# Kernel tuning notes

Hardware: AMD Instinct MI355X
Metric: run time of the kernel (lower is better)

Reference implementation:

```python
import jax, jax.numpy as jnp
import numpy as np
import math

R, C, B, E = 64, 256, 1, 768
H, DK, F = 8, 96, 3072
EPS = 1e-5


def _ln(x, w, b):
    m = jnp.mean(x, axis=-1, keepdims=True)
    v = jnp.var(x, axis=-1, keepdims=True)
    return (x - m) / jnp.sqrt(v + EPS) * w + b


def _lin(x, w, b):
    # torch Linear: y = x @ W^T + b, W: [out, in]
    return jnp.einsum('...i,oi->...o', x, w) + b


def setup_inputs() -> dict:
    key = jax.random.key(0)
    ks = jax.random.split(key, 16)
    w = lambda k, s: jax.random.normal(k, s, dtype=jnp.float32) * 0.02
    z = lambda s: jnp.zeros(s, dtype=jnp.float32)
    o = lambda s: jnp.ones(s, dtype=jnp.float32)
    return {
        'x': jax.random.normal(ks[0], (R, C, B, E), dtype=jnp.float32),
        'ln_row_w': o((E,)), 'ln_row_b': z((E,)),
        'row_q_w': w(ks[1], (E, E)), 'row_q_b': z((E,)),
        'row_k_w': w(ks[2], (E, E)), 'row_k_b': z((E,)),
        'row_v_w': w(ks[3], (E, E)), 'row_v_b': z((E,)),
        'row_o_w': w(ks[4], (E, E)), 'row_o_b': z((E,)),
        'ln_col_w': o((E,)), 'ln_col_b': z((E,)),
        'col_q_w': w(ks[5], (E, E)), 'col_q_b': z((E,)),
        'col_k_w': w(ks[6], (E, E)), 'col_k_b': z((E,)),
        'col_v_w': w(ks[7], (E, E)), 'col_v_b': z((E,)),
        'col_o_w': w(ks[8], (E, E)), 'col_o_b': z((E,)),
        'ln_ffn_w': o((E,)), 'ln_ffn_b': z((E,)),
        'fc1_w': w(ks[9], (F, E)), 'fc1_b': z((F,)),
        'fc2_w': w(ks[10], (E, F)), 'fc2_b': z((E,)),
    }


def reference(x, ln_row_w, ln_row_b, row_q_w, row_q_b, row_k_w, row_k_b,
              row_v_w, row_v_b, row_o_w, row_o_b,
              ln_col_w, ln_col_b, col_q_w, col_q_b, col_k_w, col_k_b,
              col_v_w, col_v_b, col_o_w, col_o_b,
              ln_ffn_w, ln_ffn_b, fc1_w, fc1_b, fc2_w, fc2_b):
    r, c, n, e = x.shape  # n_rows, n_cols, batch, embed

    # ---- Row self-attention (pre-LN residual block) ----
    xn = _ln(x, ln_row_w, ln_row_b)
    scaling = (DK ** -0.5) / math.sqrt(r)  # align_scaling: extra 1/sqrt(n_rows)
    q = _lin(xn, row_q_w, row_q_b).reshape(r, c, n, H, DK) * scaling
    k = _lin(xn, row_k_w, row_k_b).reshape(r, c, n, H, DK)
    v = _lin(xn, row_v_w, row_v_b).reshape(r, c, n, H, DK)
    row_logits = jnp.einsum('rinhd,rjnhd->hnij', q, k)  # sums over rows
    row_probs = jax.nn.softmax(row_logits, axis=-1)     # [H, B, C, C]
    rc = jnp.einsum('hnij,rjnhd->rinhd', row_probs, v).reshape(r, c, n, e)
    x = x + _lin(rc, row_o_w, row_o_b)

    # ---- Column self-attention (pre-LN residual block) ----
    xn = _ln(x, ln_col_w, ln_col_b)
    q = _lin(xn, col_q_w, col_q_b).reshape(r, c, n, H, DK) * (DK ** -0.5)
    k = _lin(xn, col_k_w, col_k_b).reshape(r, c, n, H, DK)
    v = _lin(xn, col_v_w, col_v_b).reshape(r, c, n, H, DK)
    col_logits = jnp.einsum('icnhd,jcnhd->hcnij', q, k)
    col_probs = jax.nn.softmax(col_logits, axis=-1)     # [H, C, B, R, R]
    cc = jnp.einsum('hcnij,jcnhd->icnhd', col_probs, v).reshape(r, c, n, e)
    x = x + _lin(cc, col_o_w, col_o_b)

    # ---- Feed-forward (pre-LN residual block) ----
    xn = _ln(x, ln_ffn_w, ln_ffn_b)
    h = jax.nn.gelu(_lin(xn, fc1_w, fc1_b), approximate=False)
    x = x + _lin(h, fc2_w, fc2_b)

    return x, row_probs, col_probs
```

## Files before the change

kernel.cpp:

```cpp
#include <hip/hip_runtime.h>
#include <cstdint>

typedef unsigned short u16;
typedef __attribute__((ext_vector_type(8))) short short8;
typedef __attribute__((ext_vector_type(4))) short short4v;
typedef __attribute__((ext_vector_type(4))) float floatx4;

#define DEV __device__ __forceinline__

DEV float bf2f(u16 u) { union { uint32_t i; float f; } w; w.i = ((uint32_t)u) << 16; return w.f; }
DEV u16 f2bf(float f) {
  union { float f; uint32_t i; } w; w.f = f;
  uint32_t x = w.i;
  return (u16)((x + 0x7fffu + ((x >> 16) & 1u)) >> 16);
}

DEV void async_copy16(const u16* g, u16* l) {
  __builtin_amdgcn_global_load_lds(
      (const __attribute__((address_space(1))) void*)(uintptr_t)g,
      (__attribute__((address_space(3))) void*)(uint32_t)(uintptr_t)l,
      16, 0, 0);
}

__global__ __launch_bounds__(256) void cvt(const float* __restrict__ s,
                                           u16* __restrict__ d, int n) {
  const int i = (blockIdx.x * 256 + threadIdx.x) * 4;
  if (i >= n) return;
  floatx4 f = *(const floatx4*)(s + i);
  short4v o;
#pragma unroll
  for (int j = 0; j < 4; ++j) o[j] = (short)f2bf(f[j]);
  *(short4v*)(d + i) = o;
}

template<bool INF32>
__global__ __launch_bounds__(256) void ln_kernel(const void* __restrict__ in,
                                                 const float* __restrict__ w,
                                                 const float* __restrict__ b,
                                                 u16* __restrict__ out) {
  const int wid = threadIdx.x >> 6, lane = threadIdx.x & 63;
  const int row = blockIdx.x * 4 + wid;
  const size_t base = (size_t)row * 768;
  float v[12];
#pragma unroll
  for (int p = 0; p < 3; ++p) {
    const int e = p * 256 + lane * 4;
    if constexpr (INF32) {
      floatx4 f = *(const floatx4*)((const float*)in + base + e);
#pragma unroll
      for (int j = 0; j < 4; ++j) v[p * 4 + j] = f[j];
    } else {
      short4v u = *(const short4v*)((const u16*)in + base + e);
#pragma unroll
      for (int j = 0; j < 4; ++j) v[p * 4 + j] = bf2f((u16)u[j]);
    }
  }
  float s = 0.f, sq = 0.f;
#pragma unroll
  for (int i = 0; i < 12; ++i) { s += v[i]; sq += v[i] * v[i]; }
#pragma unroll
  for (int m = 1; m < 64; m <<= 1) { s += __shfl_xor(s, m); sq += __shfl_xor(sq, m); }
  const float mean = s * (1.f / 768.f);
  const float var = sq * (1.f / 768.f) - mean * mean;
  const float rstd = rsqrtf(var + 1e-5f);
#pragma unroll
  for (int p = 0; p < 3; ++p) {
    const int e = p * 256 + lane * 4;
    floatx4 wv = *(const floatx4*)(w + e);
    floatx4 bv = *(const floatx4*)(b + e);
    short4v o;
#pragma unroll
    for (int j = 0; j < 4; ++j) {
      float y = (v[p * 4 + j] - mean) * rstd * wv[j] + bv[j];
      o[j] = (short)f2bf(y);
    }
    *(short4v*)(out + base + e) = o;
  }
}

template<int AMODE, int EPI>
__global__ __launch_bounds__(256) void gemm_bt(
    const u16* __restrict__ A, const u16* __restrict__ B,
    const float* __restrict__ bias, const void* __restrict__ res,
    void* __restrict__ out, int K, int lda, int ldb,
    long long aBatch, long long bBatch, long long outBatch, int ldc, float scale) {
  __shared__ u16 lA[128 * 32];
  __shared__ u16 lB[128 * 32];
  const int t = threadIdx.x;
  const int z = blockIdx.z;
  const int m0 = blockIdx.x * 128, n0 = blockIdx.y * 128;
  const u16* Ab;
  const u16* Bb;
  int koff = 0;
  if constexpr (AMODE == 0) { Ab = A + (size_t)z * aBatch; Bb = B + (size_t)z * bBatch; }
  else if constexpr (AMODE == 1) { Ab = A + z * 96; Bb = B + z * 96; }
  else { const int h = z >> 4; Ab = A + h * 96; Bb = B + h * 96; koff = (z & 15) * 384; }

  const int krow = t >> 2;
  const int kcol = (t & 3) << 3;
  const int wid = t >> 6, lane = t & 63;
  const int wr = wid >> 1, wc = wid & 1;
  const int lrow = lane & 15, lhi = lane >> 4;

  floatx4 acc[4][4];
#pragma unroll
  for (int i = 0; i < 4; ++i)
#pragma unroll
    for (int j = 0; j < 4; ++j) acc[i][j] = (floatx4){0.f, 0.f, 0.f, 0.f};

  for (int k0 = 0; k0 < K; k0 += 32) {
#pragma unroll
    for (int i = 0; i < 2; ++i) {
      const int row = i * 64 + krow;
      const int kk = koff + k0 + kcol;
      const u16 *ga, *gb;
      if constexpr (AMODE == 0) {
        ga = Ab + (size_t)(m0 + row) * lda + kk;
        gb = Bb + (size_t)(n0 + row) * ldb + kk;
      } else {
        const int r = kk / 96, d = kk - r * 96;
        ga = Ab + (size_t)r * 196608 + (size_t)(m0 + row) * 768 + d;
        gb = Bb + (size_t)r * 196608 + (size_t)(n0 + row) * 768 + d;
      }
      async_copy16(ga, lA + i * 2048 + wid * 512);
      async_copy16(gb, lB + i * 2048 + wid * 512);
    }
    asm volatile("s_waitcnt vmcnt(0)" ::: "memory");
    __syncthreads();

    short8 af[4], bfr[4];
#pragma unroll
    for (int mi = 0; mi < 4; ++mi)
      af[mi] = *(const short8*)&lA[(wr * 64 + mi * 16 + lrow) * 32 + lhi * 8];
#pragma unroll
    for (int ni = 0; ni < 4; ++ni)
      bfr[ni] = *(const short8*)&lB[(wc * 64 + ni * 16 + lrow) * 32 + lhi * 8];
#pragma unroll
    for (int mi = 0; mi < 4; ++mi)
#pragma unroll
      for (int ni = 0; ni < 4; ++ni)
        acc[mi][ni] = __builtin_amdgcn_mfma_f32_16x16x32_bf16(af[mi], bfr[ni], acc[mi][ni], 0, 0, 0);
    __syncthreads();
  }

  const int mbase = m0 + wr * 64;
  const int nbase = n0 + wc * 64;
#pragma unroll
  for (int mi = 0; mi < 4; ++mi) {
#pragma unroll
    for (int ni = 0; ni < 4; ++ni) {
      const int n = nbase + ni * 16 + lrow;
      float bz = 0.f;
      if constexpr (EPI != 1 && EPI != 7) { if (bias) bz = bias[n]; }
#pragma unroll
      for (int r4 = 0; r4 < 4; ++r4) {
        const int m = mbase + mi * 16 + lhi * 4 + r4;
        const float val = acc[mi][ni][r4];
        if constexpr (EPI == 0) {
          ((u16*)out)[(size_t)z * outBatch + (size_t)m * ldc + n] = f2bf((val + bz) * scale);
        } else if constexpr (EPI == 1) {
          ((float*)out)[(size_t)z * outBatch + (size_t)m * ldc + n] = val;
        } else if constexpr (EPI == 2) {
          const float x = val + bz;
          ((u16*)out)[(size_t)m * ldc + n] = f2bf(0.5f * x * (1.f + erff(x * 0.70710678118f)));
        } else if constexpr (EPI == 3) {
          const float r = ((const float*)res)[(size_t)m * ldc + n];
          ((float*)out)[(size_t)m * ldc + n] = r + val + bz;
        } else if constexpr (EPI == 4) {
          const float r = ((const float*)res)[(size_t)m * ldc + n];
          ((u16*)out)[(size_t)m * ldc + n] = f2bf(r + val + bz);
        } else if constexpr (EPI == 5) {
          const float r = bf2f(((const u16*)res)[(size_t)m * ldc + n]);
          ((float*)out)[(size_t)m * ldc + n] = r + val + bz;
        } else if constexpr (EPI == 6) {
          const float r = bf2f(((const u16*)res)[(size_t)m * ldc + n]);
          ((u16*)out)[(size_t)m * ldc + n] = f2bf(r + val + bz);
        } else if constexpr (EPI == 7) {
          const int rr = n / 96, d = n - rr * 96;
          ((u16*)out)[((size_t)(rr * 256 + m)) * 768 + (size_t)z * 96 + d] = f2bf(val);
        }
      }
    }
  }
}

__global__ __launch_bounds__(256) void softmax_row(const float* __restrict__ part,
                                                   float* __restrict__ probs_f,
                                                   u16* __restrict__ probs_b) {
  const int wid = threadIdx.x >> 6, lane = threadIdx.x & 63;
  const int row = blockIdx.x * 4 + wid;
  const int h = row >> 8, i = row & 255;
  const size_t base = (size_t)h * 16 * 65536 + (size_t)i * 256 + lane * 4;
  floatx4 v = (floatx4){0.f, 0.f, 0.f, 0.f};
#pragma unroll
  for (int s16 = 0; s16 < 16; ++s16) {
    floatx4 p = *(const floatx4*)(part + base + (size_t)s16 * 65536);
#pragma unroll
    for (int j = 0; j < 4; ++j) v[j] += p[j];
  }
  float mx = fmaxf(fmaxf(v[0], v[1]), fmaxf(v[2], v[3]));
#pragma unroll
  for (int m = 1; m < 64; m <<= 1) mx = fmaxf(mx, __shfl_xor(mx, m));
  float e[4], s = 0.f;
#pragma unroll
  for (int j = 0; j < 4; ++j) { e[j] = __expf(v[j] - mx); s += e[j]; }
#pragma unroll
  for (int m = 1; m < 64; m <<= 1) s += __shfl_xor(s, m);
  const float inv = 1.f / s;
  floatx4 of;
  short4v ob;
#pragma unroll
  for (int j = 0; j < 4; ++j) {
    const float p = e[j] * inv;
    of[j] = p;
    ob[j] = (short)f2bf(p);
  }
  *(floatx4*)(probs_f + (size_t)row * 256 + lane * 4) = of;
  *(short4v*)(probs_b + (size_t)row * 256 + lane * 4) = ob;
}

__global__ __launch_bounds__(256) void pack_vt(const u16* __restrict__ v, u16* __restrict__ vt) {
  __shared__ u16 S[64][104];
  const int jb = blockIdx.x, r = blockIdx.y, h = blockIdx.z;
  const int t = threadIdx.x;
#pragma unroll
  for (int p = 0; p < 3; ++p) {
    const int cid = t + p * 256;
    const int j = cid / 12, ch = cid - j * 12;
    short8 x = *(const short8*)&v[((size_t)(r * 256 + jb * 64 + j)) * 768 + h * 96 + ch * 8];
    *(short8*)&S[j][ch * 8] = x;
  }
  __syncthreads();
#pragma unroll
  for (int p = 0; p < 3; ++p) {
    const int cid = t + p * 256;
    const int d = cid / 8, cj = cid - d * 8;
    u16 tmp[8];
#pragma unroll
    for (int m = 0; m < 8; ++m) tmp[m] = S[cj * 8 + m][d];
    *(short8*)&vt[((size_t)(h * 6144 + r * 96 + d)) * 256 + jb * 64 + cj * 8] = *(short8*)tmp;
  }
}

__global__ __launch_bounds__(256) void col_attn(const u16* __restrict__ q,
                                                const u16* __restrict__ k,
                                                const u16* __restrict__ v,
                                                float* __restrict__ probs,
                                                u16* __restrict__ ctx) {
  __shared__ u16 qs[64][104];
  __shared__ u16 ks[64][104];
  __shared__ u16 vt[96][72];
  __shared__ u16 ps[64][72];
  const int c = blockIdx.x, h = blockIdx.y;
  const int t = threadIdx.x;
#pragma unroll
  for (int p = 0; p < 3; ++p) {
    const int cid = t + p * 256;
    const int i = cid / 12, ch = cid - i * 12;
    const size_t g = ((size_t)(i * 256 + c)) * 768 + h * 96 + ch * 8;
    short8 qv = *(const short8*)(q + g);
    short8 kv = *(const short8*)(k + g);
    short8 vv = *(const short8*)(v + g);
    *(short8*)&qs[i][ch * 8] = qv;
    *(short8*)&ks[i][ch * 8] = kv;
#pragma unroll
    for (int m = 0; m < 8; ++m) vt[ch * 8 + m][i] = (u16)vv[m];
  }
  __syncthreads();
  const int lane = t & 63, wid = t >> 6;
  const int lrow = lane & 15, lhi = lane >> 4;

  floatx4 s[4];
#pragma unroll
  for (int nj = 0; nj < 4; ++nj) s[nj] = (floatx4){0.f, 0.f, 0.f, 0.f};
#pragma unroll
  for (int kk = 0; kk < 3; ++kk) {
    short8 a = *(const short8*)&qs[wid * 16 + lrow][kk * 32 + lhi * 8];
#pragma unroll
    for (int nj = 0; nj < 4; ++nj) {
      short8 bb = *(const short8*)&ks[nj * 16 + lrow][kk * 32 + lhi * 8];
      s[nj] = __builtin_amdgcn_mfma_f32_16x16x32_bf16(a, bb, s[nj], 0, 0, 0);
    }
  }
  const size_t pb = ((size_t)(h * 256 + c)) * 4096;
#pragma unroll
  for (int r4 = 0; r4 < 4; ++r4) {
    float mx = fmaxf(fmaxf(s[0][r4], s[1][r4]), fmaxf(s[2][r4], s[3][r4]));
    mx = fmaxf(mx, __shfl_xor(mx, 1));
    mx = fmaxf(mx, __shfl_xor(mx, 2));
    mx = fmaxf(mx, __shfl_xor(mx, 4));
    mx = fmaxf(mx, __shfl_xor(mx, 8));
    float e[4], sum = 0.f;
#pragma unroll
    for (int nj = 0; nj < 4; ++nj) { e[nj] = __expf(s[nj][r4] - mx); sum += e[nj]; }
    sum += __shfl_xor(sum, 1);
    sum += __shfl_xor(sum, 2);
    sum += __shfl_xor(sum, 4);
    sum += __shfl_xor(sum, 8);
    const float inv = 1.f / sum;
    const int i = wid * 16 + lhi * 4 + r4;
#pragma unroll
    for (int nj = 0; nj < 4; ++nj) {
      const float pv = e[nj] * inv;
      const int j = nj * 16 + lrow;
      probs[pb + (size_t)i * 64 + j] = pv;
      ps[i][j] = f2bf(pv);
    }
  }
  __syncthreads();
  floatx4 o[6];
#pragma unroll
  for (int df = 0; df < 6; ++df) o[df] = (floatx4){0.f, 0.f, 0.f, 0.f};
#pragma unroll
  for (int k2 = 0; k2 < 2; ++k2) {
    short8 a = *(const short8*)&ps[wid * 16 + lrow][k2 * 32 + lhi * 8];
#pragma unroll
    for (int df = 0; df < 6; ++df) {
      short8 bb = *(const short8*)&vt[df * 16 + lrow][k2 * 32 + lhi * 8];
      o[df] = __builtin_amdgcn_mfma_f32_16x16x32_bf16(a, bb, o[df], 0, 0, 0);
    }
  }
#pragma unroll
  for (int df = 0; df < 6; ++df)
#pragma unroll
    for (int r4 = 0; r4 < 4; ++r4) {
      const int i = wid * 16 + lhi * 4 + r4;
      const int d = df * 16 + lrow;
      ctx[((size_t)(i * 256 + c)) * 768 + h * 96 + d] = f2bf(o[df][r4]);
    }
}

extern "C" void kernel_launch(void* const* d_in, const int* in_sizes, int n_in,
                              void* d_out, int out_size, void* d_ws, size_t ws_size,
                              hipStream_t stream) {
  const float* x_in  = (const float*)d_in[0];
  const float* lnr_w = (const float*)d_in[1];
  const float* lnr_b = (const float*)d_in[2];
  const float* rq_w  = (const float*)d_in[3];
  const float* rq_b  = (const float*)d_in[4];
  const float* rk_w  = (const float*)d_in[5];
  const float* rk_b  = (const float*)d_in[6];
  const float* rv_w  = (const float*)d_in[7];
  const float* rv_b  = (const float*)d_in[8];
  const float* ro_w  = (const float*)d_in[9];
  const float* ro_b  = (const float*)d_in[10];
  const float* lnc_w = (const float*)d_in[11];
  const float* lnc_b = (const float*)d_in[12];
  const float* cq_w  = (const float*)d_in[13];
  const float* cq_b  = (const float*)d_in[14];
  const float* ck_w  = (const float*)d_in[15];
  const float* ck_b  = (const float*)d_in[16];
  const float* cv_w  = (const float*)d_in[17];
  const float* cv_b  = (const float*)d_in[18];
  const float* co_w  = (const float*)d_in[19];
  const float* co_b  = (const float*)d_in[20];
  const float* lnf_w = (const float*)d_in[21];
  const float* lnf_b = (const float*)d_in[22];
  const float* f1_w  = (const float*)d_in[23];
  const float* f1_b  = (const float*)d_in[24];
  const float* f2_w  = (const float*)d_in[25];
  const float* f2_b  = (const float*)d_in[26];

  char* ws = (char*)d_ws;
  const size_t WSZ_E = 589824 * 2;
  u16* w_rq = (u16*)ws;
  u16* w_rk = (u16*)(ws + WSZ_E);
  u16* w_rv = (u16*)(ws + 2 * WSZ_E);
  u16* w_ro = (u16*)(ws + 3 * WSZ_E);
  u16* w_cq = (u16*)(ws + 4 * WSZ_E);
  u16* w_ck = (u16*)(ws + 5 * WSZ_E);
  u16* w_cv = (u16*)(ws + 6 * WSZ_E);
  u16* w_co = (u16*)(ws + 7 * WSZ_E);
  u16* w_f1 = (u16*)(ws + 8 * WSZ_E);
  u16* w_f2 = (u16*)(ws + 8 * WSZ_E + 4718592);
  size_t off = 8 * WSZ_E + 2 * 4718592;

  const bool xf32 = ws_size >= 147849216ULL;
  char* x_cur = ws + off;
  off += xf32 ? 50331648 : 25165824;
  u16* qb = (u16*)(ws + off); off += 25165824;
  u16* kb = (u16*)(ws + off); off += 25165824;
  u16* vb = (u16*)(ws + off); off += 25165824;
  u16* probsb = (u16*)(ws + off);

  u16* vt     = qb;
  u16* ctx1   = kb;
  u16* hidden = qb;
  u16* xn3    = vb;

  float* out_x  = (float*)d_out;
  float* out_rp = out_x + 12582912;
  float* out_cp = out_x + 13107200;
  u16* xn   = (u16*)out_x;
  u16* ctx2 = (u16*)((char*)out_x + 25165824);
  float* part = out_x;

  const dim3 blk(256);
  const float s_row = 0.0127577591f;
  const float s_col = 0.1020620726f;

  cvt<<<576, blk, 0, stream>>>(rq_w, w_rq, 589824);
  cvt<<<576, blk, 0, stream>>>(rk_w, w_rk, 589824);
  cvt<<<576, blk, 0, stream>>>(rv_w, w_rv, 589824);
  cvt<<<576, blk, 0, stream>>>(ro_w, w_ro, 589824);
  cvt<<<576, blk, 0, stream>>>(cq_w, w_cq, 589824);
  cvt<<<576, blk, 0, stream>>>(ck_w, w_ck, 589824);
  cvt<<<576, blk, 0, stream>>>(cv_w, w_cv, 589824);
  cvt<<<576, blk, 0, stream>>>(co_w, w_co, 589824);
  cvt<<<2304, blk, 0, stream>>>(f1_w, w_f1, 2359296);
  cvt<<<2304, blk, 0, stream>>>(f2_w, w_f2, 2359296);

  ln_kernel<true><<<4096, blk, 0, stream>>>(x_in, lnr_w, lnr_b, xn);
  gemm_bt<0, 0><<<dim3(128, 6, 1), blk, 0, stream>>>(xn, w_rq, rq_b, nullptr, qb, 768, 768, 768, 0, 0, 0, 768, s_row);
  gemm_bt<0, 0><<<dim3(128, 6, 1), blk, 0, stream>>>(xn, w_rk, rk_b, nullptr, kb, 768, 768, 768, 0, 0, 0, 768, 1.f);
  gemm_bt<0, 0><<<dim3(128, 6, 1), blk, 0, stream>>>(xn, w_rv, rv_b, nullptr, vb, 768, 768, 768, 0, 0, 0, 768, 1.f);
  gemm_bt<2, 1><<<dim3(2, 2, 128), blk, 0, stream>>>(qb, kb, nullptr, nullptr, part, 384, 0, 0, 0, 0, 65536LL, 256, 1.f);
  softmax_row<<<512, blk, 0, stream>>>(part, out_rp, probsb);
  pack_vt<<<dim3(4, 64, 8), blk, 0, stream>>>(vb, vt);
  gemm_bt<0, 7><<<dim3(2, 48, 8), blk, 0, stream>>>(probsb, vt, nullptr, nullptr, ctx1, 256, 256, 256, 65536LL, 1572864LL, 0, 0, 1.f);
  if (xf32)
    gemm_bt<0, 3><<<dim3(128, 6, 1), blk, 0, stream>>>(ctx1, w_ro, ro_b, x_in, x_cur, 768, 768, 768, 0, 0, 0, 768, 1.f);
  else
    gemm_bt<0, 4><<<dim3(128, 6, 1), blk, 0, stream>>>(ctx1, w_ro, ro_b, x_in, x_cur, 768, 768, 768, 0, 0, 0, 768, 1.f);

  if (xf32) ln_kernel<true><<<4096, blk, 0, stream>>>(x_cur, lnc_w, lnc_b, xn);
  else      ln_kernel<false><<<4096, blk, 0, stream>>>(x_cur, lnc_w, lnc_b, xn);
  gemm_bt<0, 0><<<dim3(128, 6, 1), blk, 0, stream>>>(xn, w_cq, cq_b, nullptr, qb, 768, 768, 768, 0, 0, 0, 768, s_col);
  gemm_bt<0, 0><<<dim3(128, 6, 1), blk, 0, stream>>>(xn, w_ck, ck_b, nullptr, kb, 768, 768, 768, 0, 0, 0, 768, 1.f);
  gemm_bt<0, 0><<<dim3(128, 6, 1), blk, 0, stream>>>(xn, w_cv, cv_b, nullptr, vb, 768, 768, 768, 0, 0, 0, 768, 1.f);
  col_attn<<<dim3(256, 8), blk, 0, stream>>>(qb, kb, vb, out_cp, ctx2);
  if (xf32)
    gemm_bt<0, 3><<<dim3(128, 6, 1), blk, 0, stream>>>(ctx2, w_co, co_b, x_cur, x_cur, 768, 768, 768, 0, 0, 0, 768, 1.f);
  else
    gemm_bt<0, 6><<<dim3(128, 6, 1), blk, 0, stream>>>(ctx2, w_co, co_b, x_cur, x_cur, 768, 768, 768, 0, 0, 0, 768, 1.f);

  if (xf32) ln_kernel<true><<<4096, blk, 0, stream>>>(x_cur, lnf_w, lnf_b, xn3);
  else      ln_kernel<false><<<4096, blk, 0, stream>>>(x_cur, lnf_w, lnf_b, xn3);
  gemm_bt<0, 2><<<dim3(128, 12, 1), blk, 0, stream>>>(xn3, w_f1, f1_b, nullptr, hidden, 768, 768, 768, 0, 0, 0, 1536, 1.f);
  if (xf32)
    gemm_bt<0, 3><<<dim3(128, 6, 1), blk, 0, stream>>>(hidden, w_f2, f2_b, x_cur, out_x, 1536, 1536, 3072, 0, 0, 0, 768, 1.f);
  else
    gemm_bt<0, 5><<<dim3(128, 6, 1), blk, 0, stream>>>(hidden, w_f2, f2_b, x_cur, out_x, 1536, 1536, 3072, 0, 0, 0, 768, 1.f);
  gemm_bt<0, 2><<<dim3(128, 12, 1), blk, 0, stream>>>(xn3, w_f1 + 1536 * 768, f1_b + 1536, nullptr, hidden, 768, 768, 768, 0, 0, 0, 1536, 1.f);
  gemm_bt<0, 3><<<dim3(128, 6, 1), blk, 0, stream>>>(hidden, w_f2 + 1536, nullptr, out_x, out_x, 1536, 1536, 3072, 0, 0, 0, 768, 1.f);
}
```

Before: 703.6 us.

## Fuse QKV GEMMs, merge weight conversions, widen GEMM K-tile, use fast GELU

Merges the ten weight-conversion launches into one kernel and folds the query scaling into the converted Q weights and packed biases. Replaces the three separate Q/K/V projection GEMMs with one wide GEMM (N=2304) whose epilogue scatters results into the q/k/v buffers. Doubles the GEMM K-tile from 32 to 64, halving the barriers per K step at the cost of twice the LDS. Swaps erff in the GELU epilogue for a polynomial approximation with fast exp, which slightly changes numerics.

Result: slower. 828.6 us (+17.8%).

```diff
diff --git a/kernel.cpp b/kernel.cpp
--- a/kernel.cpp
+++ b/kernel.cpp
@@ -15,6 +15,17 @@
   return (u16)((x + 0x7fffu + ((x >> 16) & 1u)) >> 16);
 }
 
+DEV float fast_gelu(float x) {
+  const float y = x * 0.70710678118f;
+  const float ay = fabsf(y);
+  const float t = 1.f / (1.f + 0.3275911f * ay);
+  const float poly = t * (0.254829592f + t * (-0.284496736f +
+                     t * (1.421413741f + t * (-1.453152027f + t * 1.061405429f))));
+  const float er = 1.f - poly * __expf(-y * y);
+  const float erf_y = __builtin_copysignf(er, y);
+  return 0.5f * x * (1.f + erf_y);
+}
+
 DEV void async_copy16(const u16* g, u16* l) {
   __builtin_amdgcn_global_load_lds(
       (const __attribute__((address_space(1))) void*)(uintptr_t)g,
@@ -22,15 +33,34 @@
       16, 0, 0);
 }
 
-__global__ __launch_bounds__(256) void cvt(const float* __restrict__ s,
-                                           u16* __restrict__ d, int n) {
-  const int i = (blockIdx.x * 256 + threadIdx.x) * 4;
-  if (i >= n) return;
-  floatx4 f = *(const floatx4*)(s + i);
+struct CvtArgs {
+  const float* src[10];
+  float scale[10];
+};
+__global__ __launch_bounds__(256) void cvt_all(CvtArgs a, u16* __restrict__ dst) {
+  const size_t e = ((size_t)blockIdx.x * 256 + threadIdx.x) * 4;
+  if (e >= 9437184) return;
+  int reg;
+  size_t base;
+  if (e < 4718592) { reg = (int)(e / 589824); base = (size_t)reg * 589824; }
+  else if (e < 7077888) { reg = 8; base = 4718592; }
+  else { reg = 9; base = 7077888; }
+  const float sc = a.scale[reg];
+  floatx4 f = *(const floatx4*)(a.src[reg] + (e - base));
   short4v o;
 #pragma unroll
-  for (int j = 0; j < 4; ++j) o[j] = (short)f2bf(f[j]);
-  *(short4v*)(d + i) = o;
+  for (int j = 0; j < 4; ++j) o[j] = (short)f2bf(f[j] * sc);
+  *(short4v*)(dst + e) = o;
+}
+
+__global__ __launch_bounds__(256) void bias_pack(const float* __restrict__ qb,
+                                                 const float* __restrict__ kb,
+                                                 const float* __restrict__ vb,
+                                                 float sq, float* __restrict__ out) {
+  const int i = blockIdx.x * 256 + threadIdx.x;
+  if (i >= 2304) return;
+  const int buf = i / 768, c = i - buf * 768;
+  out[i] = buf == 0 ? qb[c] * sq : (buf == 1 ? kb[c] : vb[c]);
 }
 
 template<bool INF32>
@@ -84,8 +114,8 @@
     const float* __restrict__ bias, const void* __restrict__ res,
     void* __restrict__ out, int K, int lda, int ldb,
     long long aBatch, long long bBatch, long long outBatch, int ldc, float scale) {
-  __shared__ u16 lA[128 * 32];
-  __shared__ u16 lB[128 * 32];
+  __shared__ u16 lA[128 * 64];
+  __shared__ u16 lB[128 * 64];
   const int t = threadIdx.x;
   const int z = blockIdx.z;
   const int m0 = blockIdx.x * 128, n0 = blockIdx.y * 128;
@@ -96,8 +126,8 @@
   else if constexpr (AMODE == 1) { Ab = A + z * 96; Bb = B + z * 96; }
   else { const int h = z >> 4; Ab = A + h * 96; Bb = B + h * 96; koff = (z & 15) * 384; }
 
-  const int krow = t >> 2;
-  const int kcol = (t & 3) << 3;
+  const int srow = t >> 3;
+  const int scol = (t & 7) << 3;
   const int wid = t >> 6, lane = t & 63;
   const int wr = wid >> 1, wc = wid & 1;
   const int lrow = lane & 15, lhi = lane >> 4;
@@ -108,11 +138,11 @@
 #pragma unroll
     for (int j = 0; j < 4; ++j) acc[i][j] = (floatx4){0.f, 0.f, 0.f, 0.f};
 
-  for (int k0 = 0; k0 < K; k0 += 32) {
-#pragma unroll
-    for (int i = 0; i < 2; ++i) {
-      const int row = i * 64 + krow;
-      const int kk = koff + k0 + kcol;
+  for (int k0 = 0; k0 < K; k0 += 64) {
+#pragma unroll
+    for (int p = 0; p < 4; ++p) {
+      const int row = p * 32 + srow;
+      const int kk = koff + k0 + scol;
       const u16 *ga, *gb;
       if constexpr (AMODE == 0) {
         ga = Ab + (size_t)(m0 + row) * lda + kk;
@@ -122,24 +152,27 @@
         ga = Ab + (size_t)r * 196608 + (size_t)(m0 + row) * 768 + d;
         gb = Bb + (size_t)r * 196608 + (size_t)(n0 + row) * 768 + d;
       }
-      async_copy16(ga, lA + i * 2048 + wid * 512);
-      async_copy16(gb, lB + i * 2048 + wid * 512);
+      async_copy16(ga, lA + p * 2048 + wid * 512);
+      async_copy16(gb, lB + p * 2048 + wid * 512);
     }
     asm volatile("s_waitcnt vmcnt(0)" ::: "memory");
     __syncthreads();
 
-    short8 af[4], bfr[4];
-#pragma unroll
-    for (int mi = 0; mi < 4; ++mi)
-      af[mi] = *(const short8*)&lA[(wr * 64 + mi * 16 + lrow) * 32 + lhi * 8];
-#pragma unroll
-    for (int ni = 0; ni < 4; ++ni)
-      bfr[ni] = *(const short8*)&lB[(wc * 64 + ni * 16 + lrow) * 32 + lhi * 8];
-#pragma unroll
-    for (int mi = 0; mi < 4; ++mi)
+#pragma unroll
+    for (int kh = 0; kh < 2; ++kh) {
+      short8 af[4], bfr[4];
+#pragma unroll
+      for (int mi = 0; mi < 4; ++mi)
+        af[mi] = *(const short8*)&lA[(wr * 64 + mi * 16 + lrow) * 64 + kh * 32 + lhi * 8];
 #pragma unroll
       for (int ni = 0; ni < 4; ++ni)
-        acc[mi][ni] = __builtin_amdgcn_mfma_f32_16x16x32_bf16(af[mi], bfr[ni], acc[mi][ni], 0, 0, 0);
+        bfr[ni] = *(const short8*)&lB[(wc * 64 + ni * 16 + lrow) * 64 + kh * 32 + lhi * 8];
+#pragma unroll
+      for (int mi = 0; mi < 4; ++mi)
+#pragma unroll
+        for (int ni = 0; ni < 4; ++ni)
+          acc[mi][ni] = __builtin_amdgcn_mfma_f32_16x16x32_bf16(af[mi], bfr[ni], acc[mi][ni], 0, 0, 0);
+    }
     __syncthreads();
   }
 
@@ -156,13 +189,10 @@
       for (int r4 = 0; r4 < 4; ++r4) {
         const int m = mbase + mi * 16 + lhi * 4 + r4;
         const float val = acc[mi][ni][r4];
-        if constexpr (EPI == 0) {
-          ((u16*)out)[(size_t)z * outBatch + (size_t)m * ldc + n] = f2bf((val + bz) * scale);
-        } else if constexpr (EPI == 1) {
+        if constexpr (EPI == 1) {
           ((float*)out)[(size_t)z * outBatch + (size_t)m * ldc + n] = val;
         } else if constexpr (EPI == 2) {
-          const float x = val + bz;
-          ((u16*)out)[(size_t)m * ldc + n] = f2bf(0.5f * x * (1.f + erff(x * 0.70710678118f)));
+          ((u16*)out)[(size_t)m * ldc + n] = f2bf(fast_gelu(val + bz));
         } else if constexpr (EPI == 3) {
           const float r = ((const float*)res)[(size_t)m * ldc + n];
           ((float*)out)[(size_t)m * ldc + n] = r + val + bz;
@@ -178,6 +208,9 @@
         } else if constexpr (EPI == 7) {
           const int rr = n / 96, d = n - rr * 96;
           ((u16*)out)[((size_t)(rr * 256 + m)) * 768 + (size_t)z * 96 + d] = f2bf(val);
+        } else if constexpr (EPI == 8) {
+          const int buf = n / 768, col = n - buf * 768;
+          ((u16*)out)[(size_t)buf * 12582912 + (size_t)m * 768 + col] = f2bf(val + bz);
         }
       }
     }
@@ -361,18 +394,18 @@
   const float* f2_w  = (const float*)d_in[25];
   const float* f2_b  = (const float*)d_in[26];
 
+  const float s_row = 0.0127577591f;
+  const float s_col = 0.1020620726f;
+
   char* ws = (char*)d_ws;
   const size_t WSZ_E = 589824 * 2;
-  u16* w_rq = (u16*)ws;
-  u16* w_rk = (u16*)(ws + WSZ_E);
-  u16* w_rv = (u16*)(ws + 2 * WSZ_E);
-  u16* w_ro = (u16*)(ws + 3 * WSZ_E);
-  u16* w_cq = (u16*)(ws + 4 * WSZ_E);
-  u16* w_ck = (u16*)(ws + 5 * WSZ_E);
-  u16* w_cv = (u16*)(ws + 6 * WSZ_E);
-  u16* w_co = (u16*)(ws + 7 * WSZ_E);
-  u16* w_f1 = (u16*)(ws + 8 * WSZ_E);
-  u16* w_f2 = (u16*)(ws + 8 * WSZ_E + 4718592);
+  u16* w_all = (u16*)ws;
+  u16* w_rqkv = w_all;
+  u16* w_ro   = (u16*)(ws + 3 * WSZ_E);
+  u16* w_cqkv = (u16*)(ws + 4 * WSZ_E);
+  u16* w_co   = (u16*)(ws + 7 * WSZ_E);
+  u16* w_f1   = (u16*)(ws + 8 * WSZ_E);
+  u16* w_f2   = (u16*)(ws + 8 * WSZ_E + 4718592);
   size_t off = 8 * WSZ_E + 2 * 4718592;
 
   const bool xf32 = ws_size >= 147849216ULL;
@@ -381,7 +414,9 @@
   u16* qb = (u16*)(ws + off); off += 25165824;
   u16* kb = (u16*)(ws + off); off += 25165824;
   u16* vb = (u16*)(ws + off); off += 25165824;
-  u16* probsb = (u16*)(ws + off);
+  u16* probsb = (u16*)(ws + off); off += 1048576;
+  float* qkvb_row = (float*)(ws + off); off += 9216;
+  float* qkvb_col = (float*)(ws + off); off += 9216;
 
   u16* vt     = qb;
   u16* ctx1   = kb;
@@ -396,24 +431,19 @@
   float* part = out_x;
 
   const dim3 blk(256);
-  const float s_row = 0.0127577591f;
-  const float s_col = 0.1020620726f;
-
-  cvt<<<576, blk, 0, stream>>>(rq_w, w_rq, 589824);
-  cvt<<<576, blk, 0, stream>>>(rk_w, w_rk, 589824);
-  cvt<<<576, blk, 0, stream>>>(rv_w, w_rv, 589824);
-  cvt<<<576, blk, 0, stream>>>(ro_w, w_ro, 589824);
-  cvt<<<576, blk, 0, stream>>>(cq_w, w_cq, 589824);
-  cvt<<<576, blk, 0, stream>>>(ck_w, w_ck, 589824);
-  cvt<<<576, blk, 0, stream>>>(cv_w, w_cv, 589824);
-  cvt<<<576, blk, 0, stream>>>(co_w, w_co, 589824);
-  cvt<<<2304, blk, 0, stream>>>(f1_w, w_f1, 2359296);
-  cvt<<<2304, blk, 0, stream>>>(f2_w, w_f2, 2359296);
+
+  CvtArgs ca;
+  ca.src[0] = rq_w; ca.src[1] = rk_w; ca.src[2] = rv_w; ca.src[3] = ro_w;
+  ca.src[4] = cq_w; ca.src[5] = ck_w; ca.src[6] = cv_w; ca.src[7] = co_w;
+  ca.src[8] = f1_w; ca.src[9] = f2_w;
+  for (int i = 0; i < 10; ++i) ca.scale[i] = 1.f;
+  ca.scale[0] = s_row; ca.scale[4] = s_col;
+  cvt_all<<<9216, blk, 0, stream>>>(ca, w_all);
+  bias_pack<<<9, blk, 0, stream>>>(rq_b, rk_b, rv_b, s_row, qkvb_row);
+  bias_pack<<<9, blk, 0, stream>>>(cq_b, ck_b, cv_b, s_col, qkvb_col);
 
   ln_kernel<true><<<4096, blk, 0, stream>>>(x_in, lnr_w, lnr_b, xn);
-  gemm_bt<0, 0><<<dim3(128, 6, 1), blk, 0, stream>>>(xn, w_rq, rq_b, nullptr, qb, 768, 768, 768, 0, 0, 0, 768, s_row);
-  gemm_bt<0, 0><<<dim3(128, 6, 1), blk, 0, stream>>>(xn, w_rk, rk_b, nullptr, kb, 768, 768, 768, 0, 0, 0, 768, 1.f);
-  gemm_bt<0, 0><<<dim3(128, 6, 1), blk, 0, stream>>>(xn, w_rv, rv_b, nullptr, vb, 768, 768, 768, 0, 0, 0, 768, 1.f);
+  gemm_bt<0, 8><<<dim3(128, 18, 1), blk, 0, stream>>>(xn, w_rqkv, qkvb_row, nullptr, qb, 768, 768, 768, 0, 0, 0, 768, 1.f);
   gemm_bt<2, 1><<<dim3(2, 2, 128), blk, 0, stream>>>(qb, kb, nullptr, nullptr, part, 384, 0, 0, 0, 0, 65536LL, 256, 1.f);
   softmax_row<<<512, blk, 0, stream>>>(part, out_rp, probsb);
   pack_vt<<<dim3(4, 64, 8), blk, 0, stream>>>(vb, vt);
@@ -425,9 +455,7 @@
 
   if (xf32) ln_kernel<true><<<4096, blk, 0, stream>>>(x_cur, lnc_w, lnc_b, xn);
   else      ln_kernel<false><<<4096, blk, 0, stream>>>(x_cur, lnc_w, lnc_b, xn);
-  gemm_bt<0, 0><<<dim3(128, 6, 1), blk, 0, stream>>>(xn, w_cq, cq_b, nullptr, qb, 768, 768, 768, 0, 0, 0, 768, s_col);
-  gemm_bt<0, 0><<<dim3(128, 6, 1), blk, 0, stream>>>(xn, w_ck, ck_b, nullptr, kb, 768, 768, 768, 0, 0, 0, 768, 1.f);
-  gemm_bt<0, 0><<<dim3(128, 6, 1), blk, 0, stream>>>(xn, w_cv, cv_b, nullptr, vb, 768, 768, 768, 0, 0, 0, 768, 1.f);
+  gemm_bt<0, 8><<<dim3(128, 18, 1), blk, 0, stream>>>(xn, w_cqkv, qkvb_col, nullptr, qb, 768, 768, 768, 0, 0, 0, 768, 1.f);
   col_attn<<<dim3(256, 8), blk, 0, stream>>>(qb, kb, vb, out_cp, ctx2);
   if (xf32)
     gemm_bt<0, 3><<<dim3(128, 6, 1), blk, 0, stream>>>(ctx2, w_co, co_b, x_cur, x_cur, 768, 768, 768, 0, 0, 0, 768, 1.f);
```
